# Kernel optimization log

Hardware: AMD Instinct MI355X
Metric: run time of the kernel (lower is better)

## Reference

```python
import jax, jax.numpy as jnp
import numpy as np
import math

DIM = 96
NUM_HEADS = 8
MLP_RATIO = 4.0

def _coord_encoding(h, w, scale, d_model):
    # matches HierarchicalCoordinateEncoding: per freq i, channels are
    # [sin(cell_y), cos(cell_y), sin(cell_x), cos(cell_x), sin(y), cos(y), sin(x), cos(x)]
    y = jnp.arange(h, dtype=jnp.float32) / (h - 1)
    x = jnp.arange(w, dtype=jnp.float32) / (w - 1)
    yy, xx = jnp.meshgrid(y, x, indexing='ij')
    yf = yy.reshape(-1)
    xf = xx.reshape(-1)
    cs = 2.0 / scale
    coords4 = jnp.stack([yf * cs, xf * cs, yf, xf], axis=-1)  # [N,4]
    nf = d_model // 8
    freqs = (2.0 ** jnp.arange(nf, dtype=jnp.float32)) * math.pi  # [nf]
    phase = coords4[:, None, :] * freqs[None, :, None]  # [N,nf,4]
    enc = jnp.stack([jnp.sin(phase), jnp.cos(phase)], axis=-1)  # [N,nf,4,2]
    return enc.reshape(h * w, nf * 8)  # [N,d_model] (d_model divisible by 8)

def _layernorm(x, g, b, eps=1e-5):
    mu = jnp.mean(x, axis=-1, keepdims=True)
    var = jnp.var(x, axis=-1, keepdims=True)
    return (x - mu) * jax.lax.rsqrt(var + eps) * g + b

def setup_inputs():
    key = jax.random.key(0)
    ks = jax.random.split(key, 8)
    B, C, H, W = 8, DIM, 96, 96
    hid = int(DIM * MLP_RATIO)
    std = 0.02
    return {
        'features': jax.random.normal(ks[0], (B, C, H, W), jnp.float32),
        'scale': 2,
        'mlp1_w1': jax.random.normal(ks[1], (2 * DIM, hid), jnp.float32) * std,
        'mlp1_b1': jnp.zeros((hid,), jnp.float32),
        'mlp1_w2': jax.random.normal(ks[2], (hid, DIM), jnp.float32) * std,
        'mlp1_b2': jnp.zeros((DIM,), jnp.float32),
        'norm1_g': jnp.ones((DIM,), jnp.float32),
        'norm1_b': jnp.zeros((DIM,), jnp.float32),
        'qkv_w': jax.random.normal(ks[3], (DIM, 3 * DIM), jnp.float32) * std,
        'proj_w': jax.random.normal(ks[4], (DIM, DIM), jnp.float32) * std,
        'proj_b': jnp.zeros((DIM,), jnp.float32),
        'norm2_g': jnp.ones((DIM,), jnp.float32),
        'norm2_b': jnp.zeros((DIM,), jnp.float32),
        'mlp2_w1': jax.random.normal(ks[5], (DIM, hid), jnp.float32) * std,
        'mlp2_b1': jnp.zeros((hid,), jnp.float32),
        'mlp2_w2': jax.random.normal(ks[6], (hid, 3), jnp.float32) * std,
        'mlp2_b2': jnp.zeros((3,), jnp.float32),
    }

def reference(features, scale, mlp1_w1, mlp1_b1, mlp1_w2, mlp1_b2, norm1_g, norm1_b, qkv_w, proj_w, proj_b, norm2_g, norm2_b, mlp2_w1, mlp2_b1, mlp2_w2, mlp2_b2):
    B, C, H_lr, W_lr = features.shape
    H, W = int(H_lr * scale), int(W_lr * scale)
    N = H * W
    nh = NUM_HEADS
    hd = C // nh
    ce = _coord_encoding(H, W, float(scale), C)  # [N,C]
    # bilinear upsample, half-pixel centers == torch align_corners=False
    feat_up = jax.image.resize(features, (B, C, H, W), method='linear')
    feat_flat = feat_up.transpose(0, 2, 3, 1).reshape(B, N, C)
    combined = jnp.concatenate([feat_flat, jnp.broadcast_to(ce[None], (B, N, C))], axis=-1)  # [B,N,2C]
    x = jax.nn.gelu(combined @ mlp1_w1 + mlp1_b1, approximate=False) @ mlp1_w2 + mlp1_b2  # [B,N,C]
    x = _layernorm(x, norm1_g, norm1_b)
    # linear attention: softmax over q feature dim and k token dim
    qkv = (x @ qkv_w).reshape(B, N, 3, nh, hd).transpose(2, 0, 3, 1, 4)  # [3,B,nh,N,hd]
    q, k, v = qkv[0], qkv[1], qkv[2]
    q = jax.nn.softmax(q, axis=-1) * (hd ** -0.5)
    k = jax.nn.softmax(k, axis=-2)
    ctx = jnp.einsum('bhnd,bhne->bhde', k, v)  # [B,nh,hd,hd]
    attn = jnp.einsum('bhnd,bhde->bhne', q, ctx)  # [B,nh,N,hd]
    attn = attn.transpose(0, 2, 1, 3).reshape(B, N, C)
    x = x + (attn @ proj_w + proj_b)
    x = _layernorm(x, norm2_g, norm2_b)
    rgb = jax.nn.gelu(x @ mlp2_w1 + mlp2_b1, approximate=False) @ mlp2_w2 + mlp2_b2  # [B,N,3]
    rgb = rgb.reshape(B, H, W, 3).transpose(0, 3, 1, 2)  # [B,3,H,W]
    return jnp.clip(jnp.tanh(rgb) * 0.5 + 0.5, 0.0, 1.0)
```

## Files before the change

### kernel.cpp

```cpp
#include <hip/hip_runtime.h>
#include <math.h>

typedef unsigned short u16;
typedef unsigned int   u32;
typedef unsigned long long u64;
typedef __bf16  bf16x8 __attribute__((ext_vector_type(8)));
typedef short   s16x8  __attribute__((ext_vector_type(8)));
typedef float   f32x4  __attribute__((ext_vector_type(4)));

#define NTOK 36864
#define TTOT (8*NTOK)

__device__ __forceinline__ f32x4 mfma16(s16x8 a, s16x8 b, f32x4 c){
  return __builtin_amdgcn_mfma_f32_16x16x32_bf16(
      __builtin_bit_cast(bf16x8, a), __builtin_bit_cast(bf16x8, b), c, 0, 0, 0);
}
__device__ __forceinline__ int swz(int row, int bc, int stride){
  return row*stride + (bc ^ ((row&7)<<4));
}
__device__ __forceinline__ u16 f2bf(float f){
  u32 u = __float_as_uint(f);
  return (u16)((u + 0x7fffu + ((u>>16)&1u)) >> 16);
}
__device__ __forceinline__ u32 pk2f(float a, float b){
  return (u32)f2bf(a) | ((u32)f2bf(b)<<16);
}
__device__ __forceinline__ u64 pk4f(float a, float b, float c, float d){
  return (u64)pk2f(a,b) | ((u64)pk2f(c,d)<<32);
}
__device__ __forceinline__ float bf2f(u16 h){ return __uint_as_float(((u32)h)<<16); }
__device__ __forceinline__ float rcp_(float x){ return __builtin_amdgcn_rcpf(x); }

__device__ __forceinline__ float gelu_(float x){
  float z = fabsf(x) * 0.70710678118654752f;
  float t = rcp_(1.0f + 0.3275911f*z);
  float poly = t*(0.254829592f + t*(-0.284496736f + t*(1.421413741f + t*(-1.453152027f + t*1.061405429f))));
  float e = __expf(-z*z);
  float erf = 1.0f - poly*e;
  erf = (x < 0.0f) ? -erf : erf;
  return 0.5f*x*(1.0f + erf);
}
__device__ __forceinline__ float tanhf_(float x){
  float e = __expf(2.0f*x);
  return 1.0f - 2.0f*rcp_(e + 1.0f);
}

#define LDSF(arr, row, kc, stride) (*(const s16x8*)((const char*)(arr) + swz((row),(kc)*2,(stride))))

__global__ void prep_w(const float* __restrict__ w1, const float* __restrict__ w2,
                       const float* __restrict__ qkvw, const float* __restrict__ projw,
                       const float* __restrict__ m2w1, const float* __restrict__ m2w2,
                       u16* __restrict__ w1t, u16* __restrict__ w2t,
                       u16* __restrict__ wqt, u16* __restrict__ wkt, u16* __restrict__ wvt,
                       u16* __restrict__ pjt, u16* __restrict__ m2w1t, u16* __restrict__ m2w2t)
{
  int i = blockIdx.x*256 + threadIdx.x;
  if (i < 73728){ int n=i/192, k=i%192; w1t[i] = f2bf(w1[k*384+n]); return; }
  i -= 73728;
  if (i < 36864){ int n=i/384, k=i%384; w2t[i] = f2bf(w2[k*96+n]); return; }
  i -= 36864;
  if (i < 9216){ int n=i/96, k=i%96; wqt[i] = f2bf(qkvw[k*288+n]); return; }
  i -= 9216;
  if (i < 9216){ int n=i/96, k=i%96; wkt[i] = f2bf(qkvw[k*288+96+n]); return; }
  i -= 9216;
  if (i < 9216){ int n=i/96, k=i%96; wvt[i] = f2bf(qkvw[k*288+192+n]); return; }
  i -= 9216;
  if (i < 9216){ int n=i/96, k=i%96; pjt[i] = f2bf(projw[k*96+n]); return; }
  i -= 9216;
  if (i < 36864){ int n=i/96, k=i%96; m2w1t[i] = f2bf(m2w1[k*384+n]); return; }
  i -= 36864;
  if (i < 6144){ int n=i/384, k=i%384; m2w2t[i] = (n<3)? f2bf(m2w2[k*3+n]) : (u16)0; return; }
}

__global__ void prep_feat(const float* __restrict__ feat, u16* __restrict__ featcl){
  __shared__ u16 t[96*100];
  const int tid = threadIdx.x;
  const int b = blockIdx.x/96, y = blockIdx.x%96;
  for (int i=tid; i<9216; i+=256){
    int c = i/96, x = i%96;
    t[c*100+x] = f2bf(feat[((size_t)(b*96+c)*96 + y)*96 + x]);
  }
  __syncthreads();
  for (int i=tid; i<9216; i+=256){
    int x = i/96, c = i%96;
    featcl[(((size_t)b*96 + y)*96 + x)*96 + c] = t[c*100+x];
  }
}

__global__ void prep_ce(u16* __restrict__ ce){
  int gid = blockIdx.x*256 + threadIdx.x;
  if (gid >= 36864*48) return;
  int n = gid/48, c2 = gid%48;
  int row = n/192, col = n%192;
  int fi = c2>>2, cs = c2&3;
  float coord = ((cs&1)==0) ? (float)row*(1.0f/191.0f) : (float)col*(1.0f/191.0f);
  float u = coord * (float)(1<<fi);
  u = u - 2.0f*floorf(u*0.5f);
  float ph = u * 3.14159265358979323846f;
  float s, c;
  __sincosf(ph, &s, &c);
  *(u32*)(ce + (size_t)n*96 + c2*2) = pk2f(s, c);
}

__global__ __launch_bounds__(256,3) void k1(
    const u16* __restrict__ featcl, const u16* __restrict__ ce,
    const u16* __restrict__ w1t, const float* __restrict__ b1,
    const u16* __restrict__ w2t, const float* __restrict__ b2,
    const float* __restrict__ g1, const float* __restrict__ be1,
    const u16* __restrict__ wkt, const u16* __restrict__ wvt,
    u16* __restrict__ x1, float* __restrict__ ctx_un)
{
  __shared__ u16 comb[64*192];
  __shared__ char scratch[26624];
  const int tid = threadIdx.x, w = tid>>6, lane = tid&63, kg = lane>>4, ln = lane&15;
  const int bi = blockIdx.x;
  const int b = bi/576, rem = bi%576, ty = rem/24, tx = rem%24;
  u16* hid  = (u16*)scratch;
  u16* ektp = (u16*)scratch;
  u16* vtp  = (u16*)(scratch + 12288);

  s16x8 afall[18];
  #pragma unroll
  for (int ks=0; ks<6; ++ks)
    #pragma unroll
    for (int nf=0; nf<3; ++nf)
      afall[ks*3+nf] = *(const s16x8*)(w1t + (size_t)(48*w+16*nf+ln)*192 + ks*32+8*kg);

  for (int i=tid; i<1024; i+=256){
    int rr = 96 + (i>>6), t = i&63;
    *(u16*)((char*)vtp + swz(rr, t*2, 128)) = (rr==96) ? (u16)0x3f80 : (u16)0;
  }

  {
    const u16* fbase = featcl + (size_t)b*884736;
    const int l = tid>>2, cg = tid&3;
    int row = ty*8 + (l>>3), col = tx*8 + (l&7);
    float fy = row*0.5f - 0.25f;
    int y0 = (int)floorf(fy); float dy = fy - (float)y0;
    int y0c = max(y0,0), y1c = min(y0+1,95);
    float fx = col*0.5f - 0.25f;
    int x0 = (int)floorf(fx); float dx = fx - (float)x0;
    int x0c = max(x0,0), x1c = min(x0+1,95);
    float w00=(1.f-dy)*(1.f-dx), w01=(1.f-dy)*dx, w10=dy*(1.f-dx), w11=dy*dx;
    const u16* p00 = fbase + (size_t)(y0c*96+x0c)*96;
    const u16* p01 = fbase + (size_t)(y0c*96+x1c)*96;
    const u16* p10 = fbase + (size_t)(y1c*96+x0c)*96;
    const u16* p11 = fbase + (size_t)(y1c*96+x1c)*96;
    #pragma unroll
    for (int j=0; j<12; ++j){
      int c2 = cg*12 + j;
      u32 u00 = *(const u32*)(p00 + c2*2), u01 = *(const u32*)(p01 + c2*2);
      u32 u10 = *(const u32*)(p10 + c2*2), u11 = *(const u32*)(p11 + c2*2);
      float a0 = w00*bf2f((u16)u00) + w01*bf2f((u16)u01)
               + w10*bf2f((u16)u10) + w11*bf2f((u16)u11);
      float a1 = w00*bf2f((u16)(u00>>16)) + w01*bf2f((u16)(u01>>16))
               + w10*bf2f((u16)(u10>>16)) + w11*bf2f((u16)(u11>>16));
      *(u32*)((char*)comb + swz(l, c2*4, 384)) = pk2f(a0, a1);
    }
  }
  for (int i=tid; i<64*12; i+=256){
    int l = i/12, sg = i%12;
    int n = (ty*8+(l>>3))*192 + tx*8 + (l&7);
    *(s16x8*)((char*)comb + swz(l, 192 + sg*16, 384)) = *(const s16x8*)(ce + (size_t)n*96 + sg*8);
  }
  __syncthreads();

  f32x4 a2[6] = {};
  #pragma unroll
  for (int h=0; h<2; ++h){
    if (h==1){
      #pragma unroll
      for (int ks=0; ks<6; ++ks)
        #pragma unroll
        for (int nf=0; nf<3; ++nf)
          afall[ks*3+nf] = *(const s16x8*)(w1t + (size_t)(192+48*w+16*nf+ln)*192 + ks*32+8*kg);
    }
    f32x4 acc[3][4] = {};
    #pragma unroll
    for (int ks=0; ks<6; ++ks){
      #pragma unroll
      for (int tf=0; tf<4; ++tf){
        s16x8 bfr = LDSF(comb, 16*tf+ln, ks*32+8*kg, 384);
        #pragma unroll
        for (int nf=0; nf<3; ++nf) acc[nf][tf] = mfma16(afall[ks*3+nf], bfr, acc[nf][tf]);
      }
    }
    s16x8 b01[12], b23[12], b45[12];
    #pragma unroll
    for (int k2=0; k2<2; ++k2)
      #pragma unroll
      for (int nf=0; nf<6; ++nf)
        b01[k2*6+nf] = *(const s16x8*)(w2t + (size_t)(16*nf+ln)*384 + 192*h + k2*32+8*kg);
    #pragma unroll
    for (int nf=0; nf<3; ++nf){
      int lc0 = 48*w + 16*nf + 4*kg;
      float4 bb = *(const float4*)(b1 + 192*h + lc0);
      #pragma unroll
      for (int tf=0; tf<4; ++tf){
        int token = 16*tf + ln;
        u64 v = pk4f(gelu_(acc[nf][tf][0]+bb.x), gelu_(acc[nf][tf][1]+bb.y),
                     gelu_(acc[nf][tf][2]+bb.z), gelu_(acc[nf][tf][3]+bb.w));
        *(u64*)((char*)hid + swz(token, lc0*2, 384)) = v;
      }
    }
    __syncthreads();
    #pragma unroll
    for (int k2=0; k2<2; ++k2)
      #pragma unroll
      for (int nf=0; nf<6; ++nf)
        b23[k2*6+nf] = *(const s16x8*)(w2t + (size_t)(16*nf+ln)*384 + 192*h + (2+k2)*32+8*kg);
    #pragma unroll
    for (int k2=0; k2<2; ++k2){
      s16x8 af = LDSF(hid, 16*w+ln, k2*32+8*kg, 384);
      #pragma unroll
      for (int nf=0; nf<6; ++nf) a2[nf] = mfma16(af, b01[k2*6+nf], a2[nf]);
    }
    #pragma unroll
    for (int k2=0; k2<2; ++k2)
      #pragma unroll
      for (int nf=0; nf<6; ++nf)
        b45[k2*6+nf] = *(const s16x8*)(w2t + (size_t)(16*nf+ln)*384 + 192*h + (4+k2)*32+8*kg);
    #pragma unroll
    for (int k2=0; k2<2; ++k2){
      s16x8 af = LDSF(hid, 16*w+ln, (2+k2)*32+8*kg, 384);
      #pragma unroll
      for (int nf=0; nf<6; ++nf) a2[nf] = mfma16(af, b23[k2*6+nf], a2[nf]);
    }
    #pragma unroll
    for (int k2=0; k2<2; ++k2){
      s16x8 af = LDSF(hid, 16*w+ln, (4+k2)*32+8*kg, 384);
      #pragma unroll
      for (int nf=0; nf<6; ++nf) a2[nf] = mfma16(af, b45[k2*6+nf], a2[nf]);
    }
    if (h==0) __syncthreads();
  }

  float gg[6], bbv[6];
  #pragma unroll
  for (int nf=0; nf<6; ++nf){
    int col = 16*nf + ln;
    float bias = b2[col];
    gg[nf] = g1[col]; bbv[nf] = be1[col];
    #pragma unroll
    for (int r=0; r<4; ++r) a2[nf][r] += bias;
  }
  __syncthreads();
  #pragma unroll
  for (int r=0; r<4; ++r){
    float s=0.f, sq=0.f;
    #pragma unroll
    for (int nf=0; nf<6; ++nf){ float v=a2[nf][r]; s+=v; sq+=v*v; }
    #pragma unroll
    for (int m=8; m; m>>=1){ s += __shfl_xor(s,m); sq += __shfl_xor(sq,m); }
    float mean = s*(1.f/96.f);
    float var  = sq*(1.f/96.f) - mean*mean;
    float rstd = rsqrtf(var + 1e-5f);
    int trow = 16*w + 4*kg + r;
    #pragma unroll
    for (int nf=0; nf<6; ++nf){
      float o = (a2[nf][r]-mean)*rstd*gg[nf] + bbv[nf];
      *(u16*)((char*)comb + swz(trow, (16*nf+ln)*2, 256)) = f2bf(o);
    }
  }
  __syncthreads();

  for (int i=tid; i<64*12; i+=256){
    int l = i/12, sg = i%12;
    s16x8 v = *(const s16x8*)((const char*)comb + swz(l, sg*16, 256));
    int n = (ty*8+(l>>3))*192 + tx*8 + (l&7);
    *(s16x8*)(x1 + ((size_t)b*NTOK + n)*96 + sg*8) = v;
  }

  {
    f32x4 ka[6] = {}, va[6] = {};
    #pragma unroll
    for (int ks=0; ks<3; ++ks){
      s16x8 wf[12];
      #pragma unroll
      for (int mf=0; mf<6; ++mf){
        wf[mf]   = *(const s16x8*)(wkt + (size_t)(16*mf+ln)*96 + ks*32+8*kg);
        wf[6+mf] = *(const s16x8*)(wvt + (size_t)(16*mf+ln)*96 + ks*32+8*kg);
      }
      s16x8 xb = LDSF(comb, 16*w+ln, ks*32+8*kg, 256);
      #pragma unroll
      for (int mf=0; mf<6; ++mf){
        ka[mf] = mfma16(wf[mf],   xb, ka[mf]);
        va[mf] = mfma16(wf[6+mf], xb, va[mf]);
      }
    }
    #pragma unroll
    for (int mf=0; mf<6; ++mf){
      #pragma unroll
      for (int r=0; r<4; ++r){
        int d = 16*mf + 4*kg + r;
        int tok = 16*w + ln;
        *(u16*)((char*)ektp + swz(d, tok*2, 128)) = f2bf(__expf(ka[mf][r]));
        *(u16*)((char*)vtp  + swz(d, tok*2, 128)) = f2bf(va[mf][r]);
      }
    }
  }
  __syncthreads();

  {
    const int tmi[20] = {0,0,1,1,1,2,2,3,3,4,4,4,5,5, 0,1,2,3,4,5};
    const int tni[20] = {0,1,0,1,2,1,2,3,4,3,4,5,4,5, 6,6,6,6,6,6};
    f32x4 c5[5] = {};
    #pragma unroll
    for (int t=0; t<20; ++t){
      if (t/5 == w){
        #pragma unroll
        for (int grp=0; grp<2; ++grp){
          s16x8 ea = LDSF(ektp, 16*tmi[t]+ln, 32*grp+8*kg, 128);
          s16x8 vb = LDSF(vtp,  16*tni[t]+ln, 32*grp+8*kg, 128);
          c5[t%5] = mfma16(ea, vb, c5[t%5]);
        }
      }
    }
    #pragma unroll
    for (int t=0; t<20; ++t){
      if (t/5 == w){
        #pragma unroll
        for (int r=0; r<4; ++r){
          int d = 16*tmi[t] + 4*kg + r;
          if (tni[t]==6){
            if (ln==0) atomicAdd(&ctx_un[(b*96+d)*112 + 96], c5[t%5][r]);
          } else {
            int e = 16*tni[t] + ln;
            if (d/12 == e/12) atomicAdd(&ctx_un[(b*96+d)*112 + e], c5[t%5][r]);
          }
        }
      }
    }
  }
}

__global__ void k2c(const float* __restrict__ ctx_un, u16* __restrict__ ctxBG){
  int i = blockIdx.x*256 + threadIdx.x;
  if (i >= 8*112*128) return;
  int b = i/14336, rr = i%14336, row = rr/128, d = rr%128;
  u16 v = 0;
  if (row < 96){
    if (d < 96 && d/12 == row/12){
      float c = ctx_un[(b*96+d)*112 + row] / ctx_un[(b*96+d)*112 + 96];
      v = f2bf(c * 0.28867513459481287f);
    }
  } else {
    int h = row - 96;
    if (d < 96 && d/12 == h) v = (u16)0x3f80;
  }
  ctxBG[(size_t)b*14336 + row*128 + d] = v;
}

__global__ __launch_bounds__(256,2) void k3(
    const u16* __restrict__ x1, const u16* __restrict__ wqt, const u16* __restrict__ ctxBG,
    const u16* __restrict__ pjt,
    const float* __restrict__ projb, const float* __restrict__ g2, const float* __restrict__ be2,
    const u16* __restrict__ m2w1t, const float* __restrict__ m2b1,
    const u16* __restrict__ m2w2t, const float* __restrict__ m2b2,
    float* __restrict__ out)
{
  __shared__ u16 bufA[128*128];
  __shared__ u16 bufB[128*128];
  __shared__ float rgbsh[3][128];
  const int tid = threadIdx.x, w = tid>>6, lane = tid&63, kg = lane>>4, ln = lane&15;
  const int bi = blockIdx.x, b = bi/288;
  const size_t t0 = (size_t)bi*128;
  const int n0 = (bi%288)*128;

  {
    s16x8 wq[18], xbv[6];
    #pragma unroll
    for (int ks=0; ks<3; ++ks)
      #pragma unroll
      for (int nf=0; nf<6; ++nf)
        wq[ks*6+nf] = *(const s16x8*)(wqt + (size_t)(16*nf+ln)*96 + ks*32+8*kg);
    #pragma unroll
    for (int tf=0; tf<2; ++tf)
      #pragma unroll
      for (int ks=0; ks<3; ++ks)
        xbv[tf*3+ks] = *(const s16x8*)(x1 + (t0 + 32*w + 16*tf + ln)*96 + ks*32+8*kg);
    f32x4 q[6][2] = {};
    #pragma unroll
    for (int ks=0; ks<3; ++ks)
      #pragma unroll
      for (int tf=0; tf<2; ++tf)
        #pragma unroll
        for (int nf=0; nf<6; ++nf)
          q[nf][tf] = mfma16(wq[ks*6+nf], xbv[tf*3+ks], q[nf][tf]);
    #pragma unroll
    for (int nf=0; nf<6; ++nf){
      #pragma unroll
      for (int tf=0; tf<2; ++tf){
        int token = 32*w + 16*tf + ln;
        u64 v = pk4f(__expf(q[nf][tf][0]), __expf(q[nf][tf][1]),
                     __expf(q[nf][tf][2]), __expf(q[nf][tf][3]));
        *(u64*)((char*)bufA + swz(token, (16*nf+4*kg)*2, 256)) = v;
      }
    }
  }

  f32x4 p[2][7] = {};
  {
    const u16* cb = ctxBG + (size_t)b*14336;
    s16x8 cbf[21];
    #pragma unroll
    for (int ks=0; ks<3; ++ks)
      #pragma unroll
      for (int nf=0; nf<7; ++nf)
        cbf[ks*7+nf] = *(const s16x8*)(cb + (size_t)(16*nf+ln)*128 + ks*32+8*kg);
    #pragma unroll
    for (int ks=0; ks<3; ++ks){
      s16x8 a[2];
      #pragma unroll
      for (int mi=0; mi<2; ++mi) a[mi] = LDSF(bufA, 16*(2*w+mi)+ln, ks*32+8*kg, 256);
      #pragma unroll
      for (int nf=0; nf<7; ++nf){
        #pragma unroll
        for (int mi=0; mi<2; ++mi) p[mi][nf] = mfma16(a[mi], cbf[ks*7+nf], p[mi][nf]);
      }
    }
  }
  f32x4 pp[2][6];
  #pragma unroll
  for (int mi=0; mi<2; ++mi)
    #pragma unroll
    for (int nf=0; nf<6; ++nf)
      #pragma unroll
      for (int r=0; r<4; ++r)
        pp[mi][nf][r] = bf2f(x1[(t0 + 16*(2*w+mi)+4*kg+r)*96 + 16*nf+ln]);
  s16x8 pjf[18];
  #pragma unroll
  for (int ks=0; ks<3; ++ks)
    #pragma unroll
    for (int nf=0; nf<6; ++nf)
      pjf[ks*6+nf] = *(const s16x8*)(pjt + (size_t)(16*nf+ln)*96 + ks*32+8*kg);
  #pragma unroll
  for (int mi=0; mi<2; ++mi){
    f32x4 inv;
    #pragma unroll
    for (int r=0; r<4; ++r) inv[r] = rcp_(p[mi][6][r]);
    #pragma unroll
    for (int nf=0; nf<6; ++nf){
      int h = (16*nf + ln) / 12;
      int src = (lane & 0x30) + h;
      #pragma unroll
      for (int r=0; r<4; ++r){
        float iv = __shfl(inv[r], src, 64);
        int trow = 16*(2*w+mi) + 4*kg + r;
        *(u16*)((char*)bufB + swz(trow, (16*nf+ln)*2, 256)) = f2bf(p[mi][nf][r] * iv);
      }
    }
  }

  #pragma unroll
  for (int ks=0; ks<3; ++ks){
    s16x8 a[2];
    #pragma unroll
    for (int mi=0; mi<2; ++mi) a[mi] = LDSF(bufB, 16*(2*w+mi)+ln, ks*32+8*kg, 256);
    #pragma unroll
    for (int nf=0; nf<6; ++nf){
      #pragma unroll
      for (int mi=0; mi<2; ++mi) pp[mi][nf] = mfma16(a[mi], pjf[ks*6+nf], pp[mi][nf]);
    }
  }
  {
    float gg[6], bbv[6], pb[6];
    #pragma unroll
    for (int nf=0; nf<6; ++nf){
      int col = 16*nf + ln;
      pb[nf] = projb[col]; gg[nf] = g2[col]; bbv[nf] = be2[col];
    }
    #pragma unroll
    for (int mi=0; mi<2; ++mi){
      #pragma unroll
      for (int r=0; r<4; ++r){
        int trow = 16*(2*w+mi)+4*kg+r;
        float vv[6]; float s=0.f, sq=0.f;
        #pragma unroll
        for (int nf=0; nf<6; ++nf){
          float v = pp[mi][nf][r] + pb[nf];
          vv[nf] = v; s += v; sq += v*v;
        }
        #pragma unroll
        for (int m=8; m; m>>=1){ s += __shfl_xor(s,m); sq += __shfl_xor(sq,m); }
        float mean = s*(1.f/96.f);
        float var  = sq*(1.f/96.f) - mean*mean;
        float rstd = rsqrtf(var + 1e-5f);
        #pragma unroll
        for (int nf=0; nf<6; ++nf){
          float o = (vv[nf]-mean)*rstd*gg[nf] + bbv[nf];
          *(u16*)((char*)bufA + swz(trow, (16*nf+ln)*2, 256)) = f2bf(o);
        }
      }
    }
  }

  f32x4 rgb[2] = {};
  for (int nc=0; nc<4; ++nc){
    s16x8 wm[18];
    #pragma unroll
    for (int ks=0; ks<3; ++ks)
      #pragma unroll
      for (int nf=0; nf<6; ++nf)
        wm[ks*6+nf] = *(const s16x8*)(m2w1t + (size_t)(nc*96+16*nf+ln)*96 + ks*32+8*kg);
    s16x8 wv2[3];
    #pragma unroll
    for (int ks=0; ks<3; ++ks)
      wv2[ks] = *(const s16x8*)(m2w2t + (size_t)ln*384 + nc*96 + ks*32 + 8*kg);
    f32x4 hh[6][2] = {};
    #pragma unroll
    for (int ks=0; ks<3; ++ks){
      #pragma unroll
      for (int tf=0; tf<2; ++tf){
        s16x8 bfr = LDSF(bufA, 32*w+16*tf+ln, ks*32+8*kg, 256);
        #pragma unroll
        for (int nf=0; nf<6; ++nf) hh[nf][tf] = mfma16(wm[ks*6+nf], bfr, hh[nf][tf]);
      }
    }
    #pragma unroll
    for (int nf=0; nf<6; ++nf){
      int hc0 = nc*96 + 16*nf + 4*kg;
      float4 bb = *(const float4*)(m2b1 + hc0);
      #pragma unroll
      for (int tf=0; tf<2; ++tf){
        int token = 32*w + 16*tf + ln;
        u64 v = pk4f(gelu_(hh[nf][tf][0]+bb.x), gelu_(hh[nf][tf][1]+bb.y),
                     gelu_(hh[nf][tf][2]+bb.z), gelu_(hh[nf][tf][3]+bb.w));
        *(u64*)((char*)bufB + swz(token, (16*nf+4*kg)*2, 256)) = v;
      }
    }
    #pragma unroll
    for (int ks=0; ks<3; ++ks){
      #pragma unroll
      for (int mi=0; mi<2; ++mi){
        s16x8 a = LDSF(bufB, 16*(2*w+mi)+ln, ks*32+8*kg, 256);
        rgb[mi] = mfma16(a, wv2[ks], rgb[mi]);
      }
    }
  }
  if (ln < 3){
    float bias = m2b2[ln];
    #pragma unroll
    for (int mi=0; mi<2; ++mi)
      #pragma unroll
      for (int r=0; r<4; ++r){
        int trow = 16*(2*w+mi)+4*kg+r;
        float v = tanhf_(rgb[mi][r] + bias)*0.5f + 0.5f;
        v = fminf(fmaxf(v, 0.f), 1.f);
        rgbsh[ln][trow] = v;
      }
  }
  __syncthreads();
  for (int i=tid; i<384; i+=256){
    int ch = i>>7, t = i&127;
    out[((size_t)(b*3+ch))*NTOK + n0 + t] = rgbsh[ch][t];
  }
}

extern "C" void kernel_launch(void* const* d_in, const int* in_sizes, int n_in,
                              void* d_out, int out_size, void* d_ws, size_t ws_size,
                              hipStream_t stream)
{
  (void)in_sizes; (void)n_in; (void)out_size; (void)ws_size;
  const float* feat  = (const float*)d_in[0];
  const float* m1w1  = (const float*)d_in[2];
  const float* m1b1  = (const float*)d_in[3];
  const float* m1w2  = (const float*)d_in[4];
  const float* m1b2  = (const float*)d_in[5];
  const float* n1g   = (const float*)d_in[6];
  const float* n1b   = (const float*)d_in[7];
  const float* qkvw  = (const float*)d_in[8];
  const float* projw = (const float*)d_in[9];
  const float* projb = (const float*)d_in[10];
  const float* n2g   = (const float*)d_in[11];
  const float* n2b   = (const float*)d_in[12];
  const float* m2w1  = (const float*)d_in[13];
  const float* m2b1  = (const float*)d_in[14];
  const float* m2w2  = (const float*)d_in[15];
  const float* m2b2  = (const float*)d_in[16];
  float* out = (float*)d_out;

  char* p = (char*)d_ws;
  auto bump = [&](size_t bytes)->char*{
    char* r = p;
    p += (bytes + 255) & ~(size_t)255;
    return r;
  };
  u16*  x1     = (u16*) bump((size_t)TTOT*96*2);
  u16*  featcl = (u16*) bump((size_t)8*96*96*96*2);
  u16*  ce     = (u16*) bump((size_t)NTOK*96*2);
  u16*  w1t    = (u16*) bump(73728*2);
  u16*  w2t    = (u16*) bump(36864*2);
  u16*  wqt    = (u16*) bump(9216*2);
  u16*  wkt    = (u16*) bump(9216*2);
  u16*  wvt    = (u16*) bump(9216*2);
  u16*  pjt    = (u16*) bump(9216*2);
  u16*  m2w1t  = (u16*) bump(36864*2);
  u16*  m2w2t  = (u16*) bump(6144*2);
  float* ctx_un= (float*)bump((size_t)8*96*112*4);
  u16*  ctxBG  = (u16*) bump((size_t)8*112*128*2);

  hipLaunchKernelGGL(prep_w, dim3(744), dim3(256), 0, stream,
                     m1w1, m1w2, qkvw, projw, m2w1, m2w2,
                     w1t, w2t, wqt, wkt, wvt, pjt, m2w1t, m2w2t);
  hipLaunchKernelGGL(prep_feat, dim3(768), dim3(256), 0, stream, feat, featcl);
  hipLaunchKernelGGL(prep_ce, dim3(6912), dim3(256), 0, stream, ce);
  hipMemsetAsync(ctx_un, 0, (size_t)8*96*112*4, stream);
  hipLaunchKernelGGL(k1, dim3(4608), dim3(256), 0, stream,
                     featcl, ce, w1t, m1b1, w2t, m1b2, n1g, n1b, wkt, wvt, x1, ctx_un);
  hipLaunchKernelGGL(k2c, dim3(448), dim3(256), 0, stream, ctx_un, ctxBG);
  hipLaunchKernelGGL(k3, dim3(2304), dim3(256), 0, stream,
                     x1, wqt, ctxBG, pjt, projb, n2g, n2b, m2w1t, m2b1, m2w2t, m2b2, out);
}
```

Baseline: 483.6 us.

## Cut register pressure in k1 and vectorize bilinear upsample loads

Weight fragments for the two MLP1 GEMMs and the K/V projection are no longer staged into large register arrays ahead of use. They are loaded just in time inside the k-step loops, and the h loop is no longer force-unrolled. The aim is fewer VGPRs so the 3-blocks-per-CU launch bound holds without spills, at the cost of less prefetch latency hiding on global weight loads. The bilinear upsample now uses integer index math with fixed 0.25/0.75 weights and 16-byte vector loads in place of 4-byte loads.

After: 483.2 us. No clear change (-0.1%).

```diff
diff --git a/kernel.cpp b/kernel.cpp
--- a/kernel.cpp
+++ b/kernel.cpp
@@ -119,13 +119,6 @@
   u16* ektp = (u16*)scratch;
   u16* vtp  = (u16*)(scratch + 12288);
 
-  s16x8 afall[18];
-  #pragma unroll
-  for (int ks=0; ks<6; ++ks)
-    #pragma unroll
-    for (int nf=0; nf<3; ++nf)
-      afall[ks*3+nf] = *(const s16x8*)(w1t + (size_t)(48*w+16*nf+ln)*192 + ks*32+8*kg);
-
   for (int i=tid; i<1024; i+=256){
     int rr = 96 + (i>>6), t = i&63;
     *(u16*)((char*)vtp + swz(rr, t*2, 128)) = (rr==96) ? (u16)0x3f80 : (u16)0;
@@ -135,27 +128,35 @@
     const u16* fbase = featcl + (size_t)b*884736;
     const int l = tid>>2, cg = tid&3;
     int row = ty*8 + (l>>3), col = tx*8 + (l&7);
-    float fy = row*0.5f - 0.25f;
-    int y0 = (int)floorf(fy); float dy = fy - (float)y0;
+    int y0 = (row-1)>>1;
     int y0c = max(y0,0), y1c = min(y0+1,95);
-    float fx = col*0.5f - 0.25f;
-    int x0 = (int)floorf(fx); float dx = fx - (float)x0;
+    float wy1 = (row&1) ? 0.25f : 0.75f;
+    float wy0 = 1.0f - wy1;
+    int x0 = (col-1)>>1;
     int x0c = max(x0,0), x1c = min(x0+1,95);
-    float w00=(1.f-dy)*(1.f-dx), w01=(1.f-dy)*dx, w10=dy*(1.f-dx), w11=dy*dx;
-    const u16* p00 = fbase + (size_t)(y0c*96+x0c)*96;
-    const u16* p01 = fbase + (size_t)(y0c*96+x1c)*96;
-    const u16* p10 = fbase + (size_t)(y1c*96+x0c)*96;
-    const u16* p11 = fbase + (size_t)(y1c*96+x1c)*96;
-    #pragma unroll
-    for (int j=0; j<12; ++j){
-      int c2 = cg*12 + j;
-      u32 u00 = *(const u32*)(p00 + c2*2), u01 = *(const u32*)(p01 + c2*2);
-      u32 u10 = *(const u32*)(p10 + c2*2), u11 = *(const u32*)(p11 + c2*2);
-      float a0 = w00*bf2f((u16)u00) + w01*bf2f((u16)u01)
-               + w10*bf2f((u16)u10) + w11*bf2f((u16)u11);
-      float a1 = w00*bf2f((u16)(u00>>16)) + w01*bf2f((u16)(u01>>16))
-               + w10*bf2f((u16)(u10>>16)) + w11*bf2f((u16)(u11>>16));
-      *(u32*)((char*)comb + swz(l, c2*4, 384)) = pk2f(a0, a1);
+    float wx1 = (col&1) ? 0.25f : 0.75f;
+    float wx0 = 1.0f - wx1;
+    float w00=wy0*wx0, w01=wy0*wx1, w10=wy1*wx0, w11=wy1*wx1;
+    const u16* p00 = fbase + (size_t)(y0c*96+x0c)*96 + cg*24;
+    const u16* p01 = fbase + (size_t)(y0c*96+x1c)*96 + cg*24;
+    const u16* p10 = fbase + (size_t)(y1c*96+x0c)*96 + cg*24;
+    const u16* p11 = fbase + (size_t)(y1c*96+x1c)*96 + cg*24;
+    #pragma unroll
+    for (int g=0; g<3; ++g){
+      s16x8 v00 = *(const s16x8*)(p00 + g*8);
+      s16x8 v01 = *(const s16x8*)(p01 + g*8);
+      s16x8 v10 = *(const s16x8*)(p10 + g*8);
+      s16x8 v11 = *(const s16x8*)(p11 + g*8);
+      #pragma unroll
+      for (int j2=0; j2<4; ++j2){
+        u32 u00 = ((const u32*)&v00)[j2], u01 = ((const u32*)&v01)[j2];
+        u32 u10 = ((const u32*)&v10)[j2], u11 = ((const u32*)&v11)[j2];
+        float a0 = w00*bf2f((u16)u00) + w01*bf2f((u16)u01)
+                 + w10*bf2f((u16)u10) + w11*bf2f((u16)u11);
+        float a1 = w00*bf2f((u16)(u00>>16)) + w01*bf2f((u16)(u01>>16))
+                 + w10*bf2f((u16)(u10>>16)) + w11*bf2f((u16)(u11>>16));
+        *(u32*)((char*)comb + swz(l, (cg*24 + g*8 + j2*2)*2, 384)) = pk2f(a0, a1);
+      }
     }
   }
   for (int i=tid; i<64*12; i+=256){
@@ -166,31 +167,21 @@
   __syncthreads();
 
   f32x4 a2[6] = {};
-  #pragma unroll
   for (int h=0; h<2; ++h){
-    if (h==1){
-      #pragma unroll
-      for (int ks=0; ks<6; ++ks)
-        #pragma unroll
-        for (int nf=0; nf<3; ++nf)
-          afall[ks*3+nf] = *(const s16x8*)(w1t + (size_t)(192+48*w+16*nf+ln)*192 + ks*32+8*kg);
-    }
     f32x4 acc[3][4] = {};
     #pragma unroll
     for (int ks=0; ks<6; ++ks){
+      s16x8 af[3];
+      #pragma unroll
+      for (int nf=0; nf<3; ++nf)
+        af[nf] = *(const s16x8*)(w1t + (size_t)(192*h+48*w+16*nf+ln)*192 + ks*32+8*kg);
       #pragma unroll
       for (int tf=0; tf<4; ++tf){
         s16x8 bfr = LDSF(comb, 16*tf+ln, ks*32+8*kg, 384);
         #pragma unroll
-        for (int nf=0; nf<3; ++nf) acc[nf][tf] = mfma16(afall[ks*3+nf], bfr, acc[nf][tf]);
-      }
-    }
-    s16x8 b01[12], b23[12], b45[12];
-    #pragma unroll
-    for (int k2=0; k2<2; ++k2)
-      #pragma unroll
-      for (int nf=0; nf<6; ++nf)
-        b01[k2*6+nf] = *(const s16x8*)(w2t + (size_t)(16*nf+ln)*384 + 192*h + k2*32+8*kg);
+        for (int nf=0; nf<3; ++nf) acc[nf][tf] = mfma16(af[nf], bfr, acc[nf][tf]);
+      }
+    }
     #pragma unroll
     for (int nf=0; nf<3; ++nf){
       int lc0 = 48*w + 16*nf + 4*kg;
@@ -205,32 +196,13 @@
     }
     __syncthreads();
     #pragma unroll
-    for (int k2=0; k2<2; ++k2)
-      #pragma unroll
-      for (int nf=0; nf<6; ++nf)
-        b23[k2*6+nf] = *(const s16x8*)(w2t + (size_t)(16*nf+ln)*384 + 192*h + (2+k2)*32+8*kg);
-    #pragma unroll
-    for (int k2=0; k2<2; ++k2){
-      s16x8 af = LDSF(hid, 16*w+ln, k2*32+8*kg, 384);
-      #pragma unroll
-      for (int nf=0; nf<6; ++nf) a2[nf] = mfma16(af, b01[k2*6+nf], a2[nf]);
-    }
-    #pragma unroll
-    for (int k2=0; k2<2; ++k2)
-      #pragma unroll
-      for (int nf=0; nf<6; ++nf)
-        b45[k2*6+nf] = *(const s16x8*)(w2t + (size_t)(16*nf+ln)*384 + 192*h + (4+k2)*32+8*kg);
-    #pragma unroll
-    for (int k2=0; k2<2; ++k2){
-      s16x8 af = LDSF(hid, 16*w+ln, (2+k2)*32+8*kg, 384);
-      #pragma unroll
-      for (int nf=0; nf<6; ++nf) a2[nf] = mfma16(af, b23[k2*6+nf], a2[nf]);
-    }
-    #pragma unroll
-    for (int k2=0; k2<2; ++k2){
-      s16x8 af = LDSF(hid, 16*w+ln, (4+k2)*32+8*kg, 384);
-      #pragma unroll
-      for (int nf=0; nf<6; ++nf) a2[nf] = mfma16(af, b45[k2*6+nf], a2[nf]);
+    for (int ks=0; ks<6; ++ks){
+      s16x8 af = LDSF(hid, 16*w+ln, ks*32+8*kg, 384);
+      #pragma unroll
+      for (int nf=0; nf<6; ++nf){
+        s16x8 bfr = *(const s16x8*)(w2t + (size_t)(16*nf+ln)*384 + 192*h + ks*32+8*kg);
+        a2[nf] = mfma16(af, bfr, a2[nf]);
+      }
     }
     if (h==0) __syncthreads();
   }
@@ -275,17 +247,13 @@
     f32x4 ka[6] = {}, va[6] = {};
     #pragma unroll
     for (int ks=0; ks<3; ++ks){
-      s16x8 wf[12];
+      s16x8 xb = LDSF(comb, 16*w+ln, ks*32+8*kg, 256);
       #pragma unroll
       for (int mf=0; mf<6; ++mf){
-        wf[mf]   = *(const s16x8*)(wkt + (size_t)(16*mf+ln)*96 + ks*32+8*kg);
-        wf[6+mf] = *(const s16x8*)(wvt + (size_t)(16*mf+ln)*96 + ks*32+8*kg);
-      }
-      s16x8 xb = LDSF(comb, 16*w+ln, ks*32+8*kg, 256);
-      #pragma unroll
-      for (int mf=0; mf<6; ++mf){
-        ka[mf] = mfma16(wf[mf],   xb, ka[mf]);
-        va[mf] = mfma16(wf[6+mf], xb, va[mf]);
+        s16x8 ak = *(const s16x8*)(wkt + (size_t)(16*mf+ln)*96 + ks*32+8*kg);
+        s16x8 av = *(const s16x8*)(wvt + (size_t)(16*mf+ln)*96 + ks*32+8*kg);
+        ka[mf] = mfma16(ak, xb, ka[mf]);
+        va[mf] = mfma16(av, xb, va[mf]);
       }
     }
     #pragma unroll
```
